# Performance work log

Hardware: AMD Instinct MI355X
Metric: run time of the kernel (lower is better)

## Reference

```python
import jax, jax.numpy as jnp
import numpy as np

L = 4        # number of layers
D = 4096     # square weight dim (chained matmuls require square weights)
B = 16       # rows of x (small -> weight-streaming / memory-bound)


def setup_inputs() -> dict:
    key = jax.random.key(0)
    k_x, k_b, k_m, k_d = jax.random.split(key, 4)
    x = jax.random.normal(k_x, (B, D), dtype=jnp.float32)
    base = jax.random.normal(k_b, (L, D, D), dtype=jnp.float32) * 0.02
    # mask is torch.where(ft >= base, 1.0, -1.0): a dense +/-1 sign tensor
    mask = jnp.where(jax.random.normal(k_m, (L, D, D)) >= 0, 1.0, -1.0).astype(jnp.float32)
    # bitdelta: one scalar per layer (init 0.5 in the original); use random positives
    bitdelta = jax.random.uniform(k_d, (L,), dtype=jnp.float32)
    return {"x": x, "base": base, "mask": mask, "bitdelta": bitdelta}


def reference(x, base, mask, bitdelta):
    # For each layer: W = base + bitdelta * mask ; x = x @ W
    def step(carry, layer):
        b, m, bd = layer  # b,m: [D,D], bd: scalar
        w = b + bd * m    # reconstruct dense weight from sign mask + scalar
        return jnp.matmul(carry, w), None

    out, _ = jax.lax.scan(step, x, (base, mask, bitdelta))
    return out
```

## Files before the change

### kernel.cpp

```cpp
#include <hip/hip_runtime.h>


#define DD 4096
#define BB 16
#define KW 16
#define NW 4
#define KC (KW * NW)
#define VEC 4
#define CT 256
#define TPB 256
#define KCHUNKS (DD / KC)
#define NCHUNKS (DD / CT)
#define OUT_ELEMS (BB * DD)

typedef float f32x4 __attribute__((ext_vector_type(4)));

__global__ __launch_bounds__(TPB)
void bitdelta_layer(const float* __restrict__ x,
                    const float* __restrict__ base,
                    const float* __restrict__ mask,
                    const float* __restrict__ bitdelta,
                    int layer,
                    float* __restrict__ part) {
    __shared__ float red[16][3 * 64];

    const int tid = threadIdx.x;
    const int l   = tid & 63;
    const int wid = __builtin_amdgcn_readfirstlane(tid >> 6);

    const int bid    = blockIdx.x;
    const int cchunk = bid & (NCHUNKS - 1);
    const int kchunk = bid >> 4;

    const int c0 = cchunk * CT + l * VEC;
    const int k0 = kchunk * KC + wid * KW;

    const float bd = bitdelta[layer];

    const float* wb = base + (size_t)k0 * DD + c0;
    const float* wm = mask + (size_t)k0 * DD + c0;
    const float* xp = x + k0;

    float acc[BB][VEC];
#pragma unroll
    for (int r = 0; r < BB; ++r)
#pragma unroll
        for (int c = 0; c < VEC; ++c) acc[r][c] = 0.0f;

    float4 b0 = *reinterpret_cast<const float4*>(wb);
    float4 b1 = *reinterpret_cast<const float4*>(wb + DD);
    float4 m0 = *reinterpret_cast<const float4*>(wm);
    float4 m1 = *reinterpret_cast<const float4*>(wm + DD);

#pragma unroll
    for (int kw = 0; kw < KW; kw += 2) {
        float4 nb0, nb1, nm0, nm1;
        if (kw + 2 < KW) {
            const float* pb = wb + (size_t)(kw + 2) * DD;
            const float* pm = wm + (size_t)(kw + 2) * DD;
            nb0 = *reinterpret_cast<const float4*>(pb);
            nb1 = *reinterpret_cast<const float4*>(pb + DD);
            nm0 = *reinterpret_cast<const float4*>(pm);
            nm1 = *reinterpret_cast<const float4*>(pm + DD);
        }

        const float w00 = fmaf(bd, m0.x, b0.x);
        const float w01 = fmaf(bd, m0.y, b0.y);
        const float w02 = fmaf(bd, m0.z, b0.z);
        const float w03 = fmaf(bd, m0.w, b0.w);
        const float w10 = fmaf(bd, m1.x, b1.x);
        const float w11 = fmaf(bd, m1.y, b1.y);
        const float w12 = fmaf(bd, m1.z, b1.z);
        const float w13 = fmaf(bd, m1.w, b1.w);

#pragma unroll
        for (int r = 0; r < BB; ++r) {
            const float xv0 = xp[r * DD + kw];
            const float xv1 = xp[r * DD + kw + 1];
            acc[r][0] = fmaf(xv0, w00, acc[r][0]);
            acc[r][1] = fmaf(xv0, w01, acc[r][1]);
            acc[r][2] = fmaf(xv0, w02, acc[r][2]);
            acc[r][3] = fmaf(xv0, w03, acc[r][3]);
            acc[r][0] = fmaf(xv1, w10, acc[r][0]);
            acc[r][1] = fmaf(xv1, w11, acc[r][1]);
            acc[r][2] = fmaf(xv1, w12, acc[r][2]);
            acc[r][3] = fmaf(xv1, w13, acc[r][3]);
        }

        if (kw + 2 < KW) { b0 = nb0; b1 = nb1; m0 = nm0; m1 = nm1; }
    }

#pragma unroll
    for (int t = 0; t < 4; ++t) {
        if (t) __syncthreads();
        if (wid != 0) {
#pragma unroll
            for (int e = 0; e < 16; ++e) {
                const int r = t * 4 + (e >> 2), c = e & 3;
                red[e][(wid - 1) * 64 + l] = acc[r][c];
            }
        }
        __syncthreads();
        if (wid == 0) {
#pragma unroll
            for (int e = 0; e < 16; ++e) {
                const int r = t * 4 + (e >> 2), c = e & 3;
                acc[r][c] += red[e][l] + red[e][64 + l] + red[e][128 + l];
            }
        }
    }

    if (wid == 0) {
        float* pp = part + (size_t)kchunk * OUT_ELEMS;
#pragma unroll
        for (int r = 0; r < BB; ++r) {
            const float4 v = make_float4(acc[r][0], acc[r][1], acc[r][2], acc[r][3]);
            *reinterpret_cast<float4*>(&pp[r * DD + c0]) = v;
        }
    }
}

__global__ __launch_bounds__(64)
void reduce_partials(const float* __restrict__ part, float* __restrict__ out) {
    const int idx = (blockIdx.x * 64 + threadIdx.x) * 4;
    f32x4 a = *reinterpret_cast<const f32x4*>(&part[idx]);
#pragma unroll
    for (int k = 1; k < KCHUNKS; ++k) {
        const f32x4 p = *reinterpret_cast<const f32x4*>(
            &part[(size_t)k * OUT_ELEMS + idx]);
        a += p;
    }
    *reinterpret_cast<f32x4*>(&out[idx]) = a;
}

extern "C" void kernel_launch(void* const* d_in, const int* in_sizes, int n_in,
                              void* d_out, int out_size, void* d_ws, size_t ws_size,
                              hipStream_t stream) {
    const float* x    = (const float*)d_in[0];
    const float* base = (const float*)d_in[1];
    const float* mask = (const float*)d_in[2];
    const float* bd   = (const float*)d_in[3];
    float* out = (float*)d_out;

    float* part = (float*)d_ws;
    float* y0   = part + (size_t)KCHUNKS * OUT_ELEMS;
    float* y1   = y0 + OUT_ELEMS;

    const size_t layer_stride = (size_t)DD * DD;
    const int    grid1 = KCHUNKS * NCHUNKS;
    const int    grid2 = OUT_ELEMS / (64 * 4);

    bitdelta_layer<<<grid1, TPB, 0, stream>>>(x, base, mask, bd, 0, part);
    reduce_partials<<<grid2, 64, 0, stream>>>(part, y0);

    bitdelta_layer<<<grid1, TPB, 0, stream>>>(y0, base + 1 * layer_stride,
                                              mask + 1 * layer_stride, bd, 1, part);
    reduce_partials<<<grid2, 64, 0, stream>>>(part, y1);

    bitdelta_layer<<<grid1, TPB, 0, stream>>>(y1, base + 2 * layer_stride,
                                              mask + 2 * layer_stride, bd, 2, part);
    reduce_partials<<<grid2, 64, 0, stream>>>(part, y0);

    bitdelta_layer<<<grid1, TPB, 0, stream>>>(y0, base + 3 * layer_stride,
                                              mask + 3 * layer_stride, bd, 3, part);
    reduce_partials<<<grid2, 64, 0, stream>>>(part, out);
}
```

Measured before the change: 140.3 us.

## Use 16 waves per block with two-level LDS reduction to cut split-K partials

Each block now has 16 waves instead of 4, so it covers a K-chunk four times longer. That cuts the number of split-K partial buffers written and later read by reduce_partials from 64 to 16. The in-block reduction becomes two-level: four groups of waves each reduce through LDS, then the group leaders combine into wave 0. In exchange the grid shrinks to 256 blocks of 1024 threads, roughly one per CU, with more barriers and LDS traffic, so latency hiding may suffer.

```diff
diff --git a/kernel.cpp b/kernel.cpp
--- a/kernel.cpp
+++ b/kernel.cpp
@@ -4,11 +4,11 @@
 #define DD 4096
 #define BB 16
 #define KW 16
-#define NW 4
+#define NW 16
 #define KC (KW * NW)
 #define VEC 4
 #define CT 256
-#define TPB 256
+#define TPB 1024
 #define KCHUNKS (DD / KC)
 #define NCHUNKS (DD / CT)
 #define OUT_ELEMS (BB * DD)
@@ -22,7 +22,7 @@
                     const float* __restrict__ bitdelta,
                     int layer,
                     float* __restrict__ part) {
-    __shared__ float red[16][3 * 64];
+    __shared__ float red[4][16][192];
 
     const int tid = threadIdx.x;
     const int l   = tid & 63;
@@ -90,32 +90,50 @@
         if (kw + 2 < KW) { b0 = nb0; b1 = nb1; m0 = nm0; m1 = nm1; }
     }
 
+    const int g   = wid >> 2;
+    const int sub = wid & 3;
 #pragma unroll
     for (int t = 0; t < 4; ++t) {
         if (t) __syncthreads();
-        if (wid != 0) {
+        if (sub != 0) {
 #pragma unroll
             for (int e = 0; e < 16; ++e) {
                 const int r = t * 4 + (e >> 2), c = e & 3;
-                red[e][(wid - 1) * 64 + l] = acc[r][c];
+                red[g][e][(sub - 1) * 64 + l] = acc[r][c];
             }
         }
         __syncthreads();
-        if (wid == 0) {
+        if (sub == 0) {
 #pragma unroll
             for (int e = 0; e < 16; ++e) {
                 const int r = t * 4 + (e >> 2), c = e & 3;
-                acc[r][c] += red[e][l] + red[e][64 + l] + red[e][128 + l];
+                acc[r][c] += red[g][e][l] + red[g][e][64 + l] + red[g][e][128 + l];
             }
         }
     }
+    __syncthreads();
+
+    float* r2 = &red[0][0][0];
+    if (sub == 0 && g != 0) {
+#pragma unroll
+        for (int e = 0; e < 64; ++e) {
+            const int r = e >> 2, c = e & 3;
+            r2[e * 192 + (g - 1) * 64 + l] = acc[r][c];
+        }
+    }
+    __syncthreads();
 
     if (wid == 0) {
+#pragma unroll
+        for (int e = 0; e < 64; ++e) {
+            const int r = e >> 2, c = e & 3;
+            acc[r][c] += r2[e * 192 + l] + r2[e * 192 + 64 + l] + r2[e * 192 + 128 + l];
+        }
         float* pp = part + (size_t)kchunk * OUT_ELEMS;
 #pragma unroll
         for (int r = 0; r < BB; ++r) {
-            const float4 v = make_float4(acc[r][0], acc[r][1], acc[r][2], acc[r][3]);
-            *reinterpret_cast<float4*>(&pp[r * DD + c0]) = v;
+            f32x4 v = { acc[r][0], acc[r][1], acc[r][2], acc[r][3] };
+            *reinterpret_cast<f32x4*>(&pp[r * DD + c0]) = v;
         }
     }
 }
```

Measured after the change: 170.6 us. +21.6%, slower.

## Split columns across waves and drop in-block LDS reduction

Applied to the files above, without the earlier changes.

Each wave now owns a distinct 256-column slice over a 32-row k-chunk instead of splitting k within a block, removing the shared-memory reduction and its barriers. Every wave writes its partials directly, doubling the number of k-chunks and the partial buffer traffic handled by the reduce kernel. The grid also shrinks in block count, trading intra-block sync cost for more global memory traffic and workspace use.

```diff
diff --git a/kernel.cpp b/kernel.cpp
--- a/kernel.cpp
+++ b/kernel.cpp
@@ -3,11 +3,9 @@
 
 #define DD 4096
 #define BB 16
-#define KW 16
-#define NW 4
-#define KC (KW * NW)
+#define KC 32
+#define CT 1024
 #define VEC 4
-#define CT 256
 #define TPB 256
 #define KCHUNKS (DD / KC)
 #define NCHUNKS (DD / CT)
@@ -22,18 +20,16 @@
                     const float* __restrict__ bitdelta,
                     int layer,
                     float* __restrict__ part) {
-    __shared__ float red[16][3 * 64];
-
     const int tid = threadIdx.x;
     const int l   = tid & 63;
     const int wid = __builtin_amdgcn_readfirstlane(tid >> 6);
 
     const int bid    = blockIdx.x;
     const int cchunk = bid & (NCHUNKS - 1);
-    const int kchunk = bid >> 4;
+    const int kchunk = bid >> 2;
 
-    const int c0 = cchunk * CT + l * VEC;
-    const int k0 = kchunk * KC + wid * KW;
+    const int c0 = cchunk * CT + wid * 256 + l * VEC;
+    const int k0 = kchunk * KC;
 
     const float bd = bitdelta[layer];
 
@@ -53,9 +49,9 @@
     float4 m1 = *reinterpret_cast<const float4*>(wm + DD);
 
 #pragma unroll
-    for (int kw = 0; kw < KW; kw += 2) {
+    for (int kw = 0; kw < KC; kw += 2) {
         float4 nb0, nb1, nm0, nm1;
-        if (kw + 2 < KW) {
+        if (kw + 2 < KC) {
             const float* pb = wb + (size_t)(kw + 2) * DD;
             const float* pm = wm + (size_t)(kw + 2) * DD;
             nb0 = *reinterpret_cast<const float4*>(pb);
@@ -87,36 +83,14 @@
             acc[r][3] = fmaf(xv1, w13, acc[r][3]);
         }
 
-        if (kw + 2 < KW) { b0 = nb0; b1 = nb1; m0 = nm0; m1 = nm1; }
+        if (kw + 2 < KC) { b0 = nb0; b1 = nb1; m0 = nm0; m1 = nm1; }
     }
 
+    float* pp = part + (size_t)kchunk * OUT_ELEMS + c0;
 #pragma unroll
-    for (int t = 0; t < 4; ++t) {
-        if (t) __syncthreads();
-        if (wid != 0) {
-#pragma unroll
-            for (int e = 0; e < 16; ++e) {
-                const int r = t * 4 + (e >> 2), c = e & 3;
-                red[e][(wid - 1) * 64 + l] = acc[r][c];
-            }
-        }
-        __syncthreads();
-        if (wid == 0) {
-#pragma unroll
-            for (int e = 0; e < 16; ++e) {
-                const int r = t * 4 + (e >> 2), c = e & 3;
-                acc[r][c] += red[e][l] + red[e][64 + l] + red[e][128 + l];
-            }
-        }
-    }
-
-    if (wid == 0) {
-        float* pp = part + (size_t)kchunk * OUT_ELEMS;
-#pragma unroll
-        for (int r = 0; r < BB; ++r) {
-            const float4 v = make_float4(acc[r][0], acc[r][1], acc[r][2], acc[r][3]);
-            *reinterpret_cast<float4*>(&pp[r * DD + c0]) = v;
-        }
+    for (int r = 0; r < BB; ++r) {
+        f32x4 v = { acc[r][0], acc[r][1], acc[r][2], acc[r][3] };
+        *reinterpret_cast<f32x4*>(pp + (size_t)r * DD) = v;
     }
 }
 
@@ -124,7 +98,7 @@
 void reduce_partials(const float* __restrict__ part, float* __restrict__ out) {
     const int idx = (blockIdx.x * 64 + threadIdx.x) * 4;
     f32x4 a = *reinterpret_cast<const f32x4*>(&part[idx]);
-#pragma unroll
+#pragma unroll 8
     for (int k = 1; k < KCHUNKS; ++k) {
         const f32x4 p = *reinterpret_cast<const f32x4*>(
             &part[(size_t)k * OUT_ELEMS + idx]);
```

Result: slower. 223.6 us (+59.4%).

## Fuse split-K partial reduction into layer kernel via last-block atomic counter

Applied to the files above, without the earlier changes.

Drops the separate reduce_partials launches. Each layer kernel now increments a per-column-chunk atomic counter after writing its partial, and the last block to arrive for a column chunk sums all K-chunk partials and writes that slice of the output. This removes four kernel launches and their launch gaps, and lets the reduction overlap with other blocks still running. The cost is a memset of the counters, threadfence and atomic overhead in every block, and a serial 64-deep reduction done by a single block per column chunk.

```diff
diff --git a/kernel.cpp b/kernel.cpp
--- a/kernel.cpp
+++ b/kernel.cpp
@@ -21,8 +21,11 @@
                     const float* __restrict__ mask,
                     const float* __restrict__ bitdelta,
                     int layer,
-                    float* __restrict__ part) {
+                    float* __restrict__ part,
+                    unsigned int* __restrict__ cnt,
+                    float* __restrict__ y) {
     __shared__ float red[16][3 * 64];
+    __shared__ int lastFlag;
 
     const int tid = threadIdx.x;
     const int l   = tid & 63;
@@ -114,23 +117,42 @@
         float* pp = part + (size_t)kchunk * OUT_ELEMS;
 #pragma unroll
         for (int r = 0; r < BB; ++r) {
-            const float4 v = make_float4(acc[r][0], acc[r][1], acc[r][2], acc[r][3]);
-            *reinterpret_cast<float4*>(&pp[r * DD + c0]) = v;
+            f32x4 v = { acc[r][0], acc[r][1], acc[r][2], acc[r][3] };
+            *reinterpret_cast<f32x4*>(&pp[r * DD + c0]) = v;
         }
     }
-}
 
-__global__ __launch_bounds__(64)
-void reduce_partials(const float* __restrict__ part, float* __restrict__ out) {
-    const int idx = (blockIdx.x * 64 + threadIdx.x) * 4;
-    f32x4 a = *reinterpret_cast<const f32x4*>(&part[idx]);
-#pragma unroll
-    for (int k = 1; k < KCHUNKS; ++k) {
-        const f32x4 p = *reinterpret_cast<const f32x4*>(
-            &part[(size_t)k * OUT_ELEMS + idx]);
-        a += p;
+    __syncthreads();
+    if (tid == 0) {
+        __threadfence();
+        const unsigned int old = __hip_atomic_fetch_add(
+            &cnt[cchunk], 1u, __ATOMIC_ACQ_REL, __HIP_MEMORY_SCOPE_AGENT);
+        if (old == KCHUNKS - 1) {
+            __threadfence();
+            lastFlag = 1;
+        } else {
+            lastFlag = 0;
+        }
     }
-    *reinterpret_cast<f32x4*>(&out[idx]) = a;
+    __syncthreads();
+
+    if (lastFlag) {
+        const int ft    = tid & 63;
+        const int rg    = tid >> 6;
+        const int cbase = cchunk * CT + ft * 4;
+        f32x4 s0 = 0.0f, s1 = 0.0f, s2 = 0.0f, s3 = 0.0f;
+        for (int k = 0; k < KCHUNKS; ++k) {
+            const float* ps = part + (size_t)k * OUT_ELEMS + cbase;
+            s0 += *reinterpret_cast<const f32x4*>(ps + (size_t)(rg     ) * DD);
+            s1 += *reinterpret_cast<const f32x4*>(ps + (size_t)(rg +  4) * DD);
+            s2 += *reinterpret_cast<const f32x4*>(ps + (size_t)(rg +  8) * DD);
+            s3 += *reinterpret_cast<const f32x4*>(ps + (size_t)(rg + 12) * DD);
+        }
+        *reinterpret_cast<f32x4*>(y + (size_t)(rg     ) * DD + cbase) = s0;
+        *reinterpret_cast<f32x4*>(y + (size_t)(rg +  4) * DD + cbase) = s1;
+        *reinterpret_cast<f32x4*>(y + (size_t)(rg +  8) * DD + cbase) = s2;
+        *reinterpret_cast<f32x4*>(y + (size_t)(rg + 12) * DD + cbase) = s3;
+    }
 }
 
 extern "C" void kernel_launch(void* const* d_in, const int* in_sizes, int n_in,
@@ -145,23 +167,22 @@
     float* part = (float*)d_ws;
     float* y0   = part + (size_t)KCHUNKS * OUT_ELEMS;
     float* y1   = y0 + OUT_ELEMS;
+    unsigned int* cnt = (unsigned int*)(y1 + OUT_ELEMS);
 
     const size_t layer_stride = (size_t)DD * DD;
     const int    grid1 = KCHUNKS * NCHUNKS;
-    const int    grid2 = OUT_ELEMS / (64 * 4);
 
-    bitdelta_layer<<<grid1, TPB, 0, stream>>>(x, base, mask, bd, 0, part);
-    reduce_partials<<<grid2, 64, 0, stream>>>(part, y0);
+    hipMemsetAsync(cnt, 0, 4 * NCHUNKS * sizeof(unsigned int), stream);
 
+    bitdelta_layer<<<grid1, TPB, 0, stream>>>(x, base, mask, bd, 0, part,
+                                              cnt + 0 * NCHUNKS, y0);
     bitdelta_layer<<<grid1, TPB, 0, stream>>>(y0, base + 1 * layer_stride,
-                                              mask + 1 * layer_stride, bd, 1, part);
-    reduce_partials<<<grid2, 64, 0, stream>>>(part, y1);
-
+                                              mask + 1 * layer_stride, bd, 1, part,
+                                              cnt + 1 * NCHUNKS, y1);
     bitdelta_layer<<<grid1, TPB, 0, stream>>>(y1, base + 2 * layer_stride,
-                                              mask + 2 * layer_stride, bd, 2, part);
-    reduce_partials<<<grid2, 64, 0, stream>>>(part, y0);
-
+                                              mask + 2 * layer_stride, bd, 2, part,
+                                              cnt + 2 * NCHUNKS, y0);
     bitdelta_layer<<<grid1, TPB, 0, stream>>>(y0, base + 3 * layer_stride,
-                                              mask + 3 * layer_stride, bd, 3, part);
-    reduce_partials<<<grid2, 64, 0, stream>>>(part, out);
+                                              mask + 3 * layer_stride, bd, 3, part,
+                                              cnt + 3 * NCHUNKS, out);
 }
```

Result: slower. 468.3 us (+233.8%).
